# Kernel tuning notes

Hardware: AMD Instinct MI355X
Metric: run time of the kernel (lower is better)

The kernel has to match this reference:

```python
import jax, jax.numpy as jnp
import numpy as np

DIM = 512
H = 8
D = 64
EPS = 1e-5


def _ln(x, g, b):
    m = jnp.mean(x, axis=-1, keepdims=True)
    v = jnp.var(x, axis=-1, keepdims=True)
    return (x - m) * jax.lax.rsqrt(v + EPS) * g + b


def _attn(x, ctx, wq, wk, wv, wo, bo):
    B, S, _ = x.shape
    T = ctx.shape[1]
    q = (x @ wq).reshape(B, S, H, D)
    k = (ctx @ wk).reshape(B, T, H, D)
    v = (ctx @ wv).reshape(B, T, H, D)
    scale = D ** -0.5
    score = jnp.einsum('bqhd,bkhd->bhqk', q, k) * scale  # [B,H,S,T]
    w = jax.nn.softmax(score, axis=-1)
    o = jnp.einsum('bhqk,bkhd->bqhd', w, v).reshape(B, S, H * D)
    return o @ wo + bo


def _geglu(x, w, b):
    h = x @ w + b
    y, gate = h[..., :4 * DIM], h[..., 4 * DIM:]
    tanh_res = jnp.tanh(gate * 0.7978845608 * (1.0 + 0.044715 * gate * gate))
    return y * 0.5 * gate * (1.0 + tanh_res)


def setup_inputs() -> dict:
    key = jax.random.key(0)
    ks = jax.random.split(key, 16)
    s = 0.02
    inp = {
        'x': jax.random.normal(ks[0], (2, 4096, DIM), jnp.float32),
        'context': jax.random.normal(ks[1], (2, 77, DIM), jnp.float32),
        'ln1_g': jnp.ones((DIM,), jnp.float32),
        'ln1_b': jnp.zeros((DIM,), jnp.float32),
        'wq1': jax.random.normal(ks[2], (DIM, H * D), jnp.float32) * s,
        'wk1': jax.random.normal(ks[3], (DIM, H * D), jnp.float32) * s,
        'wv1': jax.random.normal(ks[4], (DIM, H * D), jnp.float32) * s,
        'wo1': jax.random.normal(ks[5], (H * D, H * D), jnp.float32) * s,
        'bo1': jnp.zeros((H * D,), jnp.float32),
        'ln2_g': jnp.ones((DIM,), jnp.float32),
        'ln2_b': jnp.zeros((DIM,), jnp.float32),
        'wq2': jax.random.normal(ks[6], (DIM, H * D), jnp.float32) * s,
        'wk2': jax.random.normal(ks[7], (DIM, H * D), jnp.float32) * s,
        'wv2': jax.random.normal(ks[8], (DIM, H * D), jnp.float32) * s,
        'wo2': jax.random.normal(ks[9], (H * D, H * D), jnp.float32) * s,
        'bo2': jnp.zeros((H * D,), jnp.float32),
        'ln3_g': jnp.ones((DIM,), jnp.float32),
        'ln3_b': jnp.zeros((DIM,), jnp.float32),
        'geglu_w': jax.random.normal(ks[10], (DIM, 8 * DIM), jnp.float32) * s,
        'geglu_b': jnp.zeros((8 * DIM,), jnp.float32),
        'out_w': jax.random.normal(ks[11], (4 * DIM, DIM), jnp.float32) * s,
        'out_b': jnp.zeros((DIM,), jnp.float32),
    }
    return inp


def reference(x, context, ln1_g, ln1_b, wq1, wk1, wv1, wo1, bo1,
              ln2_g, ln2_b, wq2, wk2, wv2, wo2, bo2,
              ln3_g, ln3_b, geglu_w, geglu_b, out_w, out_b):
    h = _attn(_ln(x, ln1_g, ln1_b), _ln(x, ln1_g, ln1_b), wq1, wk1, wv1, wo1, bo1) + x
    h = _attn(_ln(h, ln2_g, ln2_b), context, wq2, wk2, wv2, wo2, bo2) + h
    ff = _geglu(_ln(h, ln3_g, ln3_b), geglu_w, geglu_b)
    return ff @ out_w + out_b + h
```

## Files before the change

kernel.cpp:

```cpp
#include <hip/hip_runtime.h>
#include <hip/hip_bf16.h>
#include <math.h>

#define DIM 512
#define NHEAD 8
#define HD 64
#define BATCH 2
#define SEQ 4096
#define CTXLEN 77
#define NTOK (BATCH*SEQ)
#define NCTX (BATCH*CTXLEN)

typedef __hip_bfloat16 bf16;
typedef __attribute__((ext_vector_type(8))) short bf8_t;
typedef __attribute__((ext_vector_type(4))) float f4_t;

__device__ __forceinline__ float b2f(bf16 v){ return __bfloat162float(v); }
__device__ __forceinline__ bf16  f2b(float v){ return __float2bfloat16(v); }
__device__ __forceinline__ unsigned short f2bu(float v){ bf16 h = f2b(v); return *(unsigned short*)&h; }
__device__ __forceinline__ unsigned int packbf2(float a, float b){
    return (unsigned int)f2bu(a) | ((unsigned int)f2bu(b) << 16);
}
__device__ __forceinline__ void  stf(float* p, float v){ *p = v; }
__device__ __forceinline__ void  stf(bf16* p, float v){ *p = f2b(v); }

__global__ __launch_bounds__(256)
void ln_kernel(const float* __restrict__ x, const float* __restrict__ g,
               const float* __restrict__ b, bf16* __restrict__ out, int nrows)
{
    int row  = blockIdx.x * 4 + (threadIdx.x >> 6);
    int lane = threadIdx.x & 63;
    if (row >= nrows) return;
    const float* xr = x + (size_t)row * DIM;
    float v[8];
    float s = 0.f, sq = 0.f;
    #pragma unroll
    for (int j = 0; j < 8; ++j) {
        float f = xr[lane + 64*j];
        v[j] = f; s += f; sq += f*f;
    }
    #pragma unroll
    for (int off = 32; off; off >>= 1) {
        s  += __shfl_xor(s,  off);
        sq += __shfl_xor(sq, off);
    }
    float mean = s * (1.f/DIM);
    float var  = sq * (1.f/DIM) - mean*mean;
    float rstd = rsqrtf(var + 1e-5f);
    bf16* orow = out + (size_t)row * DIM;
    #pragma unroll
    for (int j = 0; j < 8; ++j) {
        int c = lane + 64*j;
        orow[c] = f2b((v[j]-mean)*rstd*g[c] + b[c]);
    }
}

__global__ __launch_bounds__(256)
void transpose_bf16_kernel(const float* __restrict__ W, bf16* __restrict__ Wt, int K, int N)
{
    __shared__ float tile[32][33];
    int n0 = blockIdx.x * 32, k0 = blockIdx.y * 32;
    int tx = threadIdx.x & 31, ty = threadIdx.x >> 5;
    #pragma unroll
    for (int p = 0; p < 4; ++p)
        tile[ty + p*8][tx] = W[(size_t)(k0 + ty + p*8)*N + n0 + tx];
    __syncthreads();
    #pragma unroll
    for (int p = 0; p < 4; ++p)
        Wt[(size_t)(n0 + ty + p*8)*K + k0 + tx] = f2b(tile[tx][ty + p*8]);
}

struct TPtrs { const float* src[8]; bf16* dst[8]; };
__global__ __launch_bounds__(256)
void transpose8_kernel(TPtrs p)
{
    __shared__ float tile[32][33];
    const float* W = p.src[blockIdx.z];
    bf16* Wt = p.dst[blockIdx.z];
    int n0 = blockIdx.x * 32, k0 = blockIdx.y * 32;
    int tx = threadIdx.x & 31, ty = threadIdx.x >> 5;
    #pragma unroll
    for (int q = 0; q < 4; ++q)
        tile[ty + q*8][tx] = W[(size_t)(k0 + ty + q*8)*512 + n0 + tx];
    __syncthreads();
    #pragma unroll
    for (int q = 0; q < 4; ++q)
        Wt[(size_t)(n0 + ty + q*8)*512 + k0 + tx] = f2b(tile[tx][ty + q*8]);
}

__global__ __launch_bounds__(256)
void cast_bf16_kernel(const float* __restrict__ in, bf16* __restrict__ out, int n)
{
    int i = blockIdx.x*256 + threadIdx.x;
    if (i < n) out[i] = f2b(in[i]);
}

__global__ __launch_bounds__(256)
void v_transpose_kernel(const bf16* __restrict__ V, bf16* __restrict__ Vt, int T, int pitch)
{
    __shared__ __align__(16) unsigned short tile[64*64];
    const int tid = threadIdx.x;
    const int b = blockIdx.z, h = blockIdx.y;
    const int t0 = blockIdx.x * 64;
    #pragma unroll
    for (int it = 0; it < 2; ++it) {
        int e = tid + it*256;
        int t = e >> 3, c = e & 7;
        int gk = t0 + t;
        bf8_t v = {0,0,0,0,0,0,0,0};
        if (gk < T) v = *(const bf8_t*)(V + ((size_t)(b*T + gk))*DIM + h*HD + c*8);
        *(bf8_t*)&tile[t*64 + c*8] = v;
    }
    __syncthreads();
    #pragma unroll
    for (int it = 0; it < 2; ++it) {
        int e = tid + it*256;
        int d = e & 63, oc = e >> 6;
        unsigned short tmp[8];
        #pragma unroll
        for (int j = 0; j < 8; ++j) tmp[j] = tile[(oc*8 + j)*64 + d];
        *(bf8_t*)(Vt + ((size_t)((b*8 + h)*64 + d))*pitch + t0 + oc*8) = *(bf8_t*)tmp;
    }
}

struct OutPtrs { void* p[3]; };
template<int RESID, typename OUTT, bool GUARD>
__global__ __launch_bounds__(256)
void gemm_mfma_kernel(const bf16* __restrict__ A, const bf16* __restrict__ Wt,
                      const float* __restrict__ bias, const float* __restrict__ resid,
                      OutPtrs outs, int M, int K)
{
    __shared__ __align__(16) unsigned short As[128*64];
    __shared__ __align__(16) unsigned short Bs[64*64];
    const int tid  = threadIdx.x;
    const int wave = tid >> 6, lane = tid & 63;
    const int l16  = lane & 15, quad = lane >> 4;
    const int wm = (wave >> 1) * 64, wn = (wave & 1) * 32;
    const int m0 = blockIdx.y * 128, n0 = blockIdx.x * 64;
    OUTT* outp = (OUTT*)outs.p[n0 >> 9];
    const int lc0 = n0 & 511;

    f4_t acc[4][2];
    #pragma unroll
    for (int i = 0; i < 4; ++i) { acc[i][0] = f4_t{0,0,0,0}; acc[i][1] = f4_t{0,0,0,0}; }

    for (int k0 = 0; k0 < K; k0 += 64) {
        #pragma unroll
        for (int p = 0; p < 4; ++p) {
            int e = tid + p*256;
            int r = e >> 3, c = e & 7;
            int gr = m0 + r;
            if (GUARD) gr = (gr < M) ? gr : (M-1);
            bf8_t v = *(const bf8_t*)(A + (size_t)gr*K + k0 + c*8);
            *(bf8_t*)&As[r*64 + ((c ^ (r&7))*8)] = v;
        }
        #pragma unroll
        for (int p = 0; p < 2; ++p) {
            int e = tid + p*256;
            int r = e >> 3, c = e & 7;
            bf8_t v = *(const bf8_t*)(Wt + (size_t)(n0 + r)*K + k0 + c*8);
            *(bf8_t*)&Bs[r*64 + ((c ^ (r&7))*8)] = v;
        }
        __syncthreads();
        #pragma unroll
        for (int kc = 0; kc < 2; ++kc) {
            const int cg = kc*4 + quad;
            bf8_t af[4], bfr[2];
            #pragma unroll
            for (int mt = 0; mt < 4; ++mt) {
                int r = wm + mt*16 + l16;
                af[mt] = *(const bf8_t*)&As[r*64 + ((cg ^ (r&7))*8)];
            }
            #pragma unroll
            for (int nt = 0; nt < 2; ++nt) {
                int r = wn + nt*16 + l16;
                bfr[nt] = *(const bf8_t*)&Bs[r*64 + ((cg ^ (r&7))*8)];
            }
            #pragma unroll
            for (int mt = 0; mt < 4; ++mt)
                #pragma unroll
                for (int nt = 0; nt < 2; ++nt)
                    acc[mt][nt] = __builtin_amdgcn_mfma_f32_16x16x32_bf16(af[mt], bfr[nt], acc[mt][nt], 0, 0, 0);
        }
        __syncthreads();
    }

    #pragma unroll
    for (int mt = 0; mt < 4; ++mt) {
        #pragma unroll
        for (int r_ = 0; r_ < 4; ++r_) {
            int row = m0 + wm + mt*16 + quad*4 + r_;
            if (GUARD && row >= M) continue;
            size_t rb = (size_t)row * 512;
            #pragma unroll
            for (int nt = 0; nt < 2; ++nt) {
                int col = lc0 + wn + nt*16 + l16;
                float v = acc[mt][nt][r_];
                if (bias) v += bias[col];
                if (RESID) v += resid[rb + col];
                stf(&outp[rb + col], v);
            }
        }
    }
}

__global__ __launch_bounds__(256)
void geglu_mfma_kernel(const bf16* __restrict__ A, const bf16* __restrict__ WtG,
                       const float* __restrict__ bias, bf16* __restrict__ outp)
{
    __shared__ __align__(16) unsigned short As[128*64];
    __shared__ __align__(16) unsigned short Bys[64*64];
    __shared__ __align__(16) unsigned short Bgs[64*64];
    const int tid  = threadIdx.x;
    const int wave = tid >> 6, lane = tid & 63;
    const int l16  = lane & 15, quad = lane >> 4;
    const int m0 = blockIdx.y * 128, n0 = blockIdx.x * 64;
    const int srow = tid >> 3, scol = tid & 7;

    f4_t accy[2][4], accg[2][4];
    #pragma unroll
    for (int i = 0; i < 2; ++i)
        #pragma unroll
        for (int j = 0; j < 4; ++j) { accy[i][j] = f4_t{0,0,0,0}; accg[i][j] = f4_t{0,0,0,0}; }

    for (int k0 = 0; k0 < DIM; k0 += 64) {
        #pragma unroll
        for (int p = 0; p < 4; ++p) {
            int r = srow + p*32;
            bf8_t v = *(const bf8_t*)(A + (size_t)(m0 + r)*DIM + k0 + scol*8);
            *(bf8_t*)&As[r*64 + ((scol ^ (r&7))*8)] = v;
        }
        #pragma unroll
        for (int p = 0; p < 2; ++p) {
            int r = srow + p*32;
            bf8_t vy = *(const bf8_t*)(WtG + (size_t)(n0 + r)*DIM + k0 + scol*8);
            bf8_t vg = *(const bf8_t*)(WtG + (size_t)(2048 + n0 + r)*DIM + k0 + scol*8);
            *(bf8_t*)&Bys[r*64 + ((scol ^ (r&7))*8)] = vy;
            *(bf8_t*)&Bgs[r*64 + ((scol ^ (r&7))*8)] = vg;
        }
        __syncthreads();
        #pragma unroll
        for (int kc = 0; kc < 2; ++kc) {
            const int cg = kc*4 + quad;
            bf8_t af[2];
            #pragma unroll
            for (int mt = 0; mt < 2; ++mt) {
                int r = wave*32 + mt*16 + l16;
                af[mt] = *(const bf8_t*)&As[r*64 + ((cg ^ (r&7))*8)];
            }
            #pragma unroll
            for (int nt = 0; nt < 4; ++nt) {
                int r = nt*16 + l16;
                bf8_t by = *(const bf8_t*)&Bys[r*64 + ((cg ^ (r&7))*8)];
                bf8_t bg = *(const bf8_t*)&Bgs[r*64 + ((cg ^ (r&7))*8)];
                #pragma unroll
                for (int mt = 0; mt < 2; ++mt) {
                    accy[mt][nt] = __builtin_amdgcn_mfma_f32_16x16x32_bf16(af[mt], by, accy[mt][nt], 0, 0, 0);
                    accg[mt][nt] = __builtin_amdgcn_mfma_f32_16x16x32_bf16(af[mt], bg, accg[mt][nt], 0, 0, 0);
                }
            }
        }
        __syncthreads();
    }

    #pragma unroll
    for (int mt = 0; mt < 2; ++mt) {
        #pragma unroll
        for (int r_ = 0; r_ < 4; ++r_) {
            int row = m0 + wave*32 + mt*16 + quad*4 + r_;
            size_t rb = (size_t)row * 2048;
            #pragma unroll
            for (int nt = 0; nt < 4; ++nt) {
                int col = n0 + nt*16 + l16;
                float y = accy[mt][nt][r_] + bias[col];
                float g = accg[mt][nt][r_] + bias[2048 + col];
                float t = tanhf(0.7978845608f*g*(1.f + 0.044715f*g*g));
                outp[rb + col] = f2b(y * 0.5f * g * (1.f + t));
            }
        }
    }
}

__global__ __launch_bounds__(256)
void attn_mfma_kernel(const bf16* __restrict__ Qm, const bf16* __restrict__ Km,
                      const bf16* __restrict__ VtG, bf16* __restrict__ Om,
                      int T, int vpitch)
{
    __shared__ __align__(16) unsigned short Ks[64*64];
    __shared__ __align__(16) unsigned short Vts[64*64];
    __shared__ __align__(16) unsigned short Ps[4][16*64];

    const int tid  = threadIdx.x;
    const int wave = tid >> 6, lane = tid & 63;
    const int l16  = lane & 15, quad = lane >> 4;
    const int b = blockIdx.z, h = blockIdx.y;
    const int qblk = blockIdx.x * 128;

    bf8_t qf[2][2];
    #pragma unroll
    for (int qn = 0; qn < 2; ++qn) {
        const bf16* qp = Qm + ((size_t)(b*SEQ + qblk + wave*32 + qn*16 + l16))*DIM + h*HD + quad*8;
        #pragma unroll
        for (int kc = 0; kc < 2; ++kc) {
            bf8_t v = *(const bf8_t*)(qp + kc*32);
            unsigned short* u = (unsigned short*)&v;
            #pragma unroll
            for (int j = 0; j < 8; ++j) {
                bf16 hv = *(bf16*)&u[j];
                u[j] = f2bu(b2f(hv) * 0.125f);
            }
            qf[qn][kc] = v;
        }
    }

    f4_t o[4][2];
    #pragma unroll
    for (int dt = 0; dt < 4; ++dt) { o[dt][0] = f4_t{0,0,0,0}; o[dt][1] = f4_t{0,0,0,0}; }
    float m_run[2] = {-1e30f, -1e30f}, l_run[2] = {0.f, 0.f};

    const int ntiles = (T + 63) >> 6;
    for (int t0 = 0; t0 < ntiles; ++t0) {
        const int kb = t0 << 6;
        #pragma unroll
        for (int it = 0; it < 2; ++it) {
            int e = tid + it*256;
            int r = e >> 3, c = e & 7;
            int gk = kb + r;
            bf8_t kv = {0,0,0,0,0,0,0,0};
            if (gk < T) kv = *(const bf8_t*)(Km + ((size_t)(b*T + gk))*DIM + h*HD + c*8);
            *(bf8_t*)&Ks[r*64 + ((c ^ (r&7))*8)] = kv;
            bf8_t vv = *(const bf8_t*)(VtG + ((size_t)((b*8 + h)*64 + r))*vpitch + kb + c*8);
            *(bf8_t*)&Vts[r*64 + ((c ^ (r&7))*8)] = vv;
        }
        __syncthreads();

        bf8_t kf[4][2], vf[4][2];
        #pragma unroll
        for (int t = 0; t < 4; ++t) {
            int r = t*16 + l16;
            #pragma unroll
            for (int kc = 0; kc < 2; ++kc) {
                int cg = kc*4 + quad;
                kf[t][kc] = *(const bf8_t*)&Ks[r*64 + ((cg ^ (r&7))*8)];
                vf[t][kc] = *(const bf8_t*)&Vts[r*64 + ((cg ^ (r&7))*8)];
            }
        }
        const bool tail = (kb + 64 > T);

        #pragma unroll
        for (int qn = 0; qn < 2; ++qn) {
            f4_t sc[4];
            #pragma unroll
            for (int km = 0; km < 4; ++km) {
                f4_t c = {0,0,0,0};
                c = __builtin_amdgcn_mfma_f32_16x16x32_bf16(kf[km][0], qf[qn][0], c, 0, 0, 0);
                c = __builtin_amdgcn_mfma_f32_16x16x32_bf16(kf[km][1], qf[qn][1], c, 0, 0, 0);
                sc[km] = c;
            }
            if (tail) {
                #pragma unroll
                for (int km = 0; km < 4; ++km)
                    #pragma unroll
                    for (int r = 0; r < 4; ++r)
                        if (kb + km*16 + quad*4 + r >= T) sc[km][r] = -1e30f;
            }
            float mx = sc[0][0];
            #pragma unroll
            for (int km = 0; km < 4; ++km)
                #pragma unroll
                for (int r = 0; r < 4; ++r) mx = fmaxf(mx, sc[km][r]);
            mx = fmaxf(mx, __shfl_xor(mx, 16));
            mx = fmaxf(mx, __shfl_xor(mx, 32));
            float mnew = fmaxf(m_run[qn], mx);
            float psum = 0.f;
            #pragma unroll
            for (int km = 0; km < 4; ++km)
                #pragma unroll
                for (int r = 0; r < 4; ++r) {
                    float p = __expf(sc[km][r] - mnew);
                    sc[km][r] = p; psum += p;
                }
            psum += __shfl_xor(psum, 16);
            psum += __shfl_xor(psum, 32);
            float alpha = __expf(m_run[qn] - mnew);
            m_run[qn] = mnew;
            l_run[qn] = l_run[qn]*alpha + psum;
            #pragma unroll
            for (int dt = 0; dt < 4; ++dt)
                #pragma unroll
                for (int r = 0; r < 4; ++r) o[dt][qn][r] *= alpha;
            #pragma unroll
            for (int km = 0; km < 4; ++km) {
                uint2 w;
                w.x = packbf2(sc[km][0], sc[km][1]);
                w.y = packbf2(sc[km][2], sc[km][3]);
                int chunk = 2*km + (quad >> 1);
                int a = l16*64 + ((chunk ^ (l16 & 7))*8) + (quad & 1)*4;
                *(uint2*)&Ps[wave][a] = w;
            }
            #pragma unroll
            for (int kc = 0; kc < 2; ++kc) {
                int cg = kc*4 + quad;
                bf8_t pf = *(const bf8_t*)&Ps[wave][l16*64 + ((cg ^ (l16 & 7))*8)];
                #pragma unroll
                for (int dt = 0; dt < 4; ++dt)
                    o[dt][qn] = __builtin_amdgcn_mfma_f32_16x16x32_bf16(vf[dt][kc], pf, o[dt][qn], 0, 0, 0);
            }
        }
        __syncthreads();
    }

    #pragma unroll
    for (int qn = 0; qn < 2; ++qn) {
        float inv = 1.f / l_run[qn];
        int tok = qblk + wave*32 + qn*16 + l16;
        size_t base = ((size_t)(b*SEQ + tok))*DIM + h*HD;
        #pragma unroll
        for (int dt = 0; dt < 4; ++dt) {
            uint2 w;
            w.x = packbf2(o[dt][qn][0]*inv, o[dt][qn][1]*inv);
            w.y = packbf2(o[dt][qn][2]*inv, o[dt][qn][3]*inv);
            *(uint2*)(Om + base + dt*16 + quad*4) = w;
        }
    }
}

extern "C" void kernel_launch(void* const* d_in, const int* in_sizes, int n_in,
                              void* d_out, int out_size, void* d_ws, size_t ws_size,
                              hipStream_t stream)
{
    (void)in_sizes; (void)n_in; (void)out_size; (void)ws_size;
    const float* x    = (const float*)d_in[0];
    const float* ctx  = (const float*)d_in[1];
    const float* ln1g = (const float*)d_in[2];
    const float* ln1b = (const float*)d_in[3];
    const float* wq1  = (const float*)d_in[4];
    const float* wk1  = (const float*)d_in[5];
    const float* wv1  = (const float*)d_in[6];
    const float* wo1  = (const float*)d_in[7];
    const float* bo1  = (const float*)d_in[8];
    const float* ln2g = (const float*)d_in[9];
    const float* ln2b = (const float*)d_in[10];
    const float* wq2  = (const float*)d_in[11];
    const float* wk2  = (const float*)d_in[12];
    const float* wv2  = (const float*)d_in[13];
    const float* wo2  = (const float*)d_in[14];
    const float* bo2  = (const float*)d_in[15];
    const float* ln3g = (const float*)d_in[16];
    const float* ln3b = (const float*)d_in[17];
    const float* gw   = (const float*)d_in[18];
    const float* gb   = (const float*)d_in[19];
    const float* ow   = (const float*)d_in[20];
    const float* ob   = (const float*)d_in[21];
    float* out = (float*)d_out;

    char* ws = (char*)d_ws;
    bf16* An  = (bf16*)(ws);
    bf16* VtG = (bf16*)(ws);
    bf16* Qb  = (bf16*)(ws + ((size_t)8<<20));
    bf16* Kb  = (bf16*)(ws + ((size_t)16<<20));
    bf16* Vb  = (bf16*)(ws + ((size_t)24<<20));
    bf16* Ob  = (bf16*)(ws + ((size_t)32<<20));
    bf16* FF  = Qb;
    float* Hf = out;
    bf16* WT  = (bf16*)(ws + ((size_t)40<<20));
    bf16* wq1T = WT + 0*262144, *wk1T = WT + 1*262144, *wv1T = WT + 2*262144, *wo1T = WT + 3*262144;
    bf16* wq2T = WT + 4*262144, *wk2T = WT + 5*262144, *wv2T = WT + 6*262144, *wo2T = WT + 7*262144;
    bf16* gwT  = (bf16*)(ws + ((size_t)44<<20));
    bf16* owT  = (bf16*)(ws + ((size_t)48<<20));
    bf16* ctxb = (bf16*)(ws + ((size_t)50<<20));
    bf16* VtG2 = (bf16*)(ws + ((size_t)50<<20) + ((size_t)512<<10));

    dim3 blk(256);

    TPtrs tp;
    tp.src[0]=wq1; tp.src[1]=wk1; tp.src[2]=wv1; tp.src[3]=wo1;
    tp.src[4]=wq2; tp.src[5]=wk2; tp.src[6]=wv2; tp.src[7]=wo2;
    tp.dst[0]=wq1T; tp.dst[1]=wk1T; tp.dst[2]=wv1T; tp.dst[3]=wo1T;
    tp.dst[4]=wq2T; tp.dst[5]=wk2T; tp.dst[6]=wv2T; tp.dst[7]=wo2T;
    transpose8_kernel<<<dim3(16,16,8), blk, 0, stream>>>(tp);
    transpose_bf16_kernel<<<dim3(128,16), blk, 0, stream>>>(gw, gwT, DIM, 4096);
    transpose_bf16_kernel<<<dim3(16,64), blk, 0, stream>>>(ow, owT, 2048, DIM);
    cast_bf16_kernel<<<dim3((NCTX*DIM+255)/256), blk, 0, stream>>>(ctx, ctxb, NCTX*DIM);

    dim3 gLN(NTOK/4);
    dim3 gQKV(24, 64);
    dim3 gG(8, 64);
    dim3 gKVx(16, 2);
    dim3 gGEGLU(32, 64);
    dim3 gATT(SEQ/128, NHEAD, BATCH);
    OutPtrs oQKV{{Qb, Kb, Vb}};
    OutPtrs oKVx{{Kb, Vb, nullptr}};
    OutPtrs oQ{{Qb, nullptr, nullptr}};
    OutPtrs oH{{Hf, nullptr, nullptr}};
    OutPtrs oOut{{out, nullptr, nullptr}};
    OutPtrs oOb{{Ob, nullptr, nullptr}};

    ln_kernel<<<gLN, blk, 0, stream>>>(x, ln1g, ln1b, An, NTOK);
    gemm_mfma_kernel<0,bf16,false><<<gQKV, blk, 0, stream>>>(An, wq1T, nullptr, nullptr, oQKV, NTOK, DIM);
    v_transpose_kernel<<<dim3(SEQ/64, NHEAD, BATCH), blk, 0, stream>>>(Vb, VtG, SEQ, SEQ);
    attn_mfma_kernel<<<gATT, blk, 0, stream>>>(Qb, Kb, VtG, Ob, SEQ, SEQ);
    gemm_mfma_kernel<1,float,false><<<gG, blk, 0, stream>>>(Ob, wo1T, bo1, x, oH, NTOK, DIM);

    ln_kernel<<<gLN, blk, 0, stream>>>(Hf, ln2g, ln2b, An, NTOK);
    gemm_mfma_kernel<0,bf16,false><<<gG, blk, 0, stream>>>(An, wq2T, nullptr, nullptr, oQ, NTOK, DIM);
    gemm_mfma_kernel<0,bf16,true><<<gKVx, blk, 0, stream>>>(ctxb, wk2T, nullptr, nullptr, oKVx, NCTX, DIM);
    v_transpose_kernel<<<dim3(2, NHEAD, BATCH), blk, 0, stream>>>(Vb, VtG2, CTXLEN, 128);
    attn_mfma_kernel<<<gATT, blk, 0, stream>>>(Qb, Kb, VtG2, Ob, CTXLEN, 128);
    gemm_mfma_kernel<1,float,false><<<gG, blk, 0, stream>>>(Ob, wo2T, bo2, Hf, oH, NTOK, DIM);

    ln_kernel<<<gLN, blk, 0, stream>>>(Hf, ln3g, ln3b, An, NTOK);
    geglu_mfma_kernel<<<gGEGLU, blk, 0, stream>>>(An, gwT, gb, FF);
    gemm_mfma_kernel<1,float,false><<<gG, blk, 0, stream>>>(FF, owT, ob, Hf, oOut, NTOK, 2048);
}
```

Measured before the change: 549.3 us.

## Split self-attention over two key halves and merge partial softmax results

The self-attention kernel now splits the key range into two halves, doubling the grid so more blocks run across the CUs. Each half writes bf16 partial outputs plus per-row running max and sum into workspace, and a new merge kernel combines them with rescaled weights. Separately, log2(e) is folded into the query scale so exp2f replaces __expf. The cost is an extra kernel launch, extra global traffic for the partials and max/sum values, and some added bf16 rounding from the intermediate partial outputs.

```diff
diff --git a/kernel.cpp b/kernel.cpp
--- a/kernel.cpp
+++ b/kernel.cpp
@@ -281,10 +281,11 @@
     }
 }
 
+template<bool FINAL>
 __global__ __launch_bounds__(256)
 void attn_mfma_kernel(const bf16* __restrict__ Qm, const bf16* __restrict__ Km,
                       const bf16* __restrict__ VtG, bf16* __restrict__ Om,
-                      int T, int vpitch)
+                      float2* __restrict__ ml, int T, int vpitch)
 {
     __shared__ __align__(16) unsigned short Ks[64*64];
     __shared__ __align__(16) unsigned short Vts[64*64];
@@ -293,7 +294,11 @@
     const int tid  = threadIdx.x;
     const int wave = tid >> 6, lane = tid & 63;
     const int l16  = lane & 15, quad = lane >> 4;
-    const int b = blockIdx.z, h = blockIdx.y;
+    const int z = blockIdx.z, h = blockIdx.y;
+    const int b = FINAL ? z : (z >> 1);
+    const int s = FINAL ? 0 : (z & 1);
+    const int kstart = FINAL ? 0 : s*(SEQ/2);
+    const int kend   = FINAL ? T : kstart + SEQ/2;
     const int qblk = blockIdx.x * 128;
 
     bf8_t qf[2][2];
@@ -307,7 +312,7 @@
             #pragma unroll
             for (int j = 0; j < 8; ++j) {
                 bf16 hv = *(bf16*)&u[j];
-                u[j] = f2bu(b2f(hv) * 0.125f);
+                u[j] = f2bu(b2f(hv) * 0.1803368801f);
             }
             qf[qn][kc] = v;
         }
@@ -318,9 +323,7 @@
     for (int dt = 0; dt < 4; ++dt) { o[dt][0] = f4_t{0,0,0,0}; o[dt][1] = f4_t{0,0,0,0}; }
     float m_run[2] = {-1e30f, -1e30f}, l_run[2] = {0.f, 0.f};
 
-    const int ntiles = (T + 63) >> 6;
-    for (int t0 = 0; t0 < ntiles; ++t0) {
-        const int kb = t0 << 6;
+    for (int kb = kstart; kb < kend; kb += 64) {
         #pragma unroll
         for (int it = 0; it < 2; ++it) {
             int e = tid + it*256;
@@ -377,12 +380,12 @@
             for (int km = 0; km < 4; ++km)
                 #pragma unroll
                 for (int r = 0; r < 4; ++r) {
-                    float p = __expf(sc[km][r] - mnew);
+                    float p = exp2f(sc[km][r] - mnew);
                     sc[km][r] = p; psum += p;
                 }
             psum += __shfl_xor(psum, 16);
             psum += __shfl_xor(psum, 32);
-            float alpha = __expf(m_run[qn] - mnew);
+            float alpha = exp2f(m_run[qn] - mnew);
             m_run[qn] = mnew;
             l_run[qn] = l_run[qn]*alpha + psum;
             #pragma unroll
@@ -410,6 +413,7 @@
         __syncthreads();
     }
 
+    bf16* Ob_ = FINAL ? Om : (Om + (size_t)s * NTOK * DIM);
     #pragma unroll
     for (int qn = 0; qn < 2; ++qn) {
         float inv = 1.f / l_run[qn];
@@ -420,9 +424,39 @@
             uint2 w;
             w.x = packbf2(o[dt][qn][0]*inv, o[dt][qn][1]*inv);
             w.y = packbf2(o[dt][qn][2]*inv, o[dt][qn][3]*inv);
-            *(uint2*)(Om + base + dt*16 + quad*4) = w;
-        }
-    }
+            *(uint2*)(Ob_ + base + dt*16 + quad*4) = w;
+        }
+        if (!FINAL && quad == 0)
+            ml[((size_t)(z*NHEAD + h))*SEQ + tok] = make_float2(m_run[qn], l_run[qn]);
+    }
+}
+
+__global__ __launch_bounds__(256)
+void attn_merge_kernel(const bf16* __restrict__ P, const float2* __restrict__ ml,
+                       bf16* __restrict__ Out)
+{
+    int idx = blockIdx.x*256 + threadIdx.x;
+    int tok = idx >> 6;
+    int c = idx & 63, h = c >> 3, dc = c & 7;
+    int b = tok >> 12, stok = tok & 4095;
+    float2 ml0 = ml[((size_t)((b*2+0)*NHEAD + h))*SEQ + stok];
+    float2 ml1 = ml[((size_t)((b*2+1)*NHEAD + h))*SEQ + stok];
+    float m = fmaxf(ml0.x, ml1.x);
+    float a0 = exp2f(ml0.x - m) * ml0.y;
+    float a1 = exp2f(ml1.x - m) * ml1.y;
+    float inv = 1.f / (a0 + a1);
+    a0 *= inv; a1 *= inv;
+    size_t off = (size_t)tok*DIM + h*HD + dc*8;
+    bf8_t v0 = *(const bf8_t*)(P + off);
+    bf8_t v1 = *(const bf8_t*)(P + (size_t)NTOK*DIM + off);
+    unsigned short r[8];
+    #pragma unroll
+    for (int j = 0; j < 8; ++j) {
+        float f0 = b2f(*(bf16*)&((unsigned short*)&v0)[j]);
+        float f1 = b2f(*(bf16*)&((unsigned short*)&v1)[j]);
+        r[j] = f2bu(a0*f0 + a1*f1);
+    }
+    *(bf8_t*)(Out + off) = *(bf8_t*)r;
 }
 
 extern "C" void kernel_launch(void* const* d_in, const int* in_sizes, int n_in,
@@ -470,6 +504,7 @@
     bf16* owT  = (bf16*)(ws + ((size_t)48<<20));
     bf16* ctxb = (bf16*)(ws + ((size_t)50<<20));
     bf16* VtG2 = (bf16*)(ws + ((size_t)50<<20) + ((size_t)512<<10));
+    float2* mlbuf = (float2*)(ws + ((size_t)51<<20));
 
     dim3 blk(256);
 
@@ -488,25 +523,26 @@
     dim3 gG(8, 64);
     dim3 gKVx(16, 2);
     dim3 gGEGLU(32, 64);
-    dim3 gATT(SEQ/128, NHEAD, BATCH);
+    dim3 gATTs(SEQ/128, NHEAD, BATCH*2);
+    dim3 gATTx(SEQ/128, NHEAD, BATCH);
     OutPtrs oQKV{{Qb, Kb, Vb}};
     OutPtrs oKVx{{Kb, Vb, nullptr}};
     OutPtrs oQ{{Qb, nullptr, nullptr}};
     OutPtrs oH{{Hf, nullptr, nullptr}};
     OutPtrs oOut{{out, nullptr, nullptr}};
-    OutPtrs oOb{{Ob, nullptr, nullptr}};
 
     ln_kernel<<<gLN, blk, 0, stream>>>(x, ln1g, ln1b, An, NTOK);
     gemm_mfma_kernel<0,bf16,false><<<gQKV, blk, 0, stream>>>(An, wq1T, nullptr, nullptr, oQKV, NTOK, DIM);
     v_transpose_kernel<<<dim3(SEQ/64, NHEAD, BATCH), blk, 0, stream>>>(Vb, VtG, SEQ, SEQ);
-    attn_mfma_kernel<<<gATT, blk, 0, stream>>>(Qb, Kb, VtG, Ob, SEQ, SEQ);
-    gemm_mfma_kernel<1,float,false><<<gG, blk, 0, stream>>>(Ob, wo1T, bo1, x, oH, NTOK, DIM);
+    attn_mfma_kernel<false><<<gATTs, blk, 0, stream>>>(Qb, Kb, VtG, Vb, mlbuf, SEQ, SEQ);
+    attn_merge_kernel<<<dim3(NTOK*NHEAD*8/256), blk, 0, stream>>>(Vb, mlbuf, Qb);
+    gemm_mfma_kernel<1,float,false><<<gG, blk, 0, stream>>>(Qb, wo1T, bo1, x, oH, NTOK, DIM);
 
     ln_kernel<<<gLN, blk, 0, stream>>>(Hf, ln2g, ln2b, An, NTOK);
     gemm_mfma_kernel<0,bf16,false><<<gG, blk, 0, stream>>>(An, wq2T, nullptr, nullptr, oQ, NTOK, DIM);
     gemm_mfma_kernel<0,bf16,true><<<gKVx, blk, 0, stream>>>(ctxb, wk2T, nullptr, nullptr, oKVx, NCTX, DIM);
     v_transpose_kernel<<<dim3(2, NHEAD, BATCH), blk, 0, stream>>>(Vb, VtG2, CTXLEN, 128);
-    attn_mfma_kernel<<<gATT, blk, 0, stream>>>(Qb, Kb, VtG2, Ob, CTXLEN, 128);
+    attn_mfma_kernel<true><<<gATTx, blk, 0, stream>>>(Qb, Kb, VtG2, Ob, nullptr, CTXLEN, 128);
     gemm_mfma_kernel<1,float,false><<<gG, blk, 0, stream>>>(Ob, wo2T, bo2, Hf, oH, NTOK, DIM);
 
     ln_kernel<<<gLN, blk, 0, stream>>>(Hf, ln3g, ln3b, An, NTOK);
```

After: 578.2 us. 1.05x slower.

## Process 128-key tiles with two independent softmax streams and exp2 scaling

Applied to the files above, without the earlier changes.

The attention kernel now loads 128 keys per iteration and splits them into two 64-key subtiles. Each subtile keeps its own running max, sum and output accumulator, and the two are merged in a final rescale. This halves the number of block barriers and gives the scheduler two independent MFMA/softmax chains. The query scale now folds in log2(e) so exp2f can replace __expf. In exchange, LDS use doubles and accumulator registers grow, which may lower occupancy, and V fragments are now read from LDS inside the PV loop instead of being preloaded.

```diff
diff --git a/kernel.cpp b/kernel.cpp
--- a/kernel.cpp
+++ b/kernel.cpp
@@ -286,9 +286,9 @@
                       const bf16* __restrict__ VtG, bf16* __restrict__ Om,
                       int T, int vpitch)
 {
-    __shared__ __align__(16) unsigned short Ks[64*64];
-    __shared__ __align__(16) unsigned short Vts[64*64];
-    __shared__ __align__(16) unsigned short Ps[4][16*64];
+    __shared__ __align__(16) unsigned short Ks[128*64];
+    __shared__ __align__(16) unsigned short Vts[64*128];
+    __shared__ __align__(16) unsigned short Ps[2][4][16*64];
 
     const int tid  = threadIdx.x;
     const int wave = tid >> 6, lane = tid & 63;
@@ -307,104 +307,116 @@
             #pragma unroll
             for (int j = 0; j < 8; ++j) {
                 bf16 hv = *(bf16*)&u[j];
-                u[j] = f2bu(b2f(hv) * 0.125f);
+                u[j] = f2bu(b2f(hv) * 0.1803368801f);
             }
             qf[qn][kc] = v;
         }
     }
 
-    f4_t o[4][2];
-    #pragma unroll
-    for (int dt = 0; dt < 4; ++dt) { o[dt][0] = f4_t{0,0,0,0}; o[dt][1] = f4_t{0,0,0,0}; }
-    float m_run[2] = {-1e30f, -1e30f}, l_run[2] = {0.f, 0.f};
-
-    const int ntiles = (T + 63) >> 6;
-    for (int t0 = 0; t0 < ntiles; ++t0) {
-        const int kb = t0 << 6;
-        #pragma unroll
-        for (int it = 0; it < 2; ++it) {
-            int e = tid + it*256;
+    f4_t o[2][4][2];
+    float m_run[2][2], l_run[2][2];
+    #pragma unroll
+    for (int st = 0; st < 2; ++st) {
+        #pragma unroll
+        for (int dt = 0; dt < 4; ++dt) { o[st][dt][0] = f4_t{0,0,0,0}; o[st][dt][1] = f4_t{0,0,0,0}; }
+        m_run[st][0] = -1e30f; m_run[st][1] = -1e30f;
+        l_run[st][0] = 0.f;    l_run[st][1] = 0.f;
+    }
+
+    const int kend = ((T + 63) >> 6) << 6;
+    for (int kb = 0; kb < kend; kb += 128) {
+        #pragma unroll
+        for (int p = 0; p < 4; ++p) {
+            int e = tid + p*256;
             int r = e >> 3, c = e & 7;
             int gk = kb + r;
             bf8_t kv = {0,0,0,0,0,0,0,0};
             if (gk < T) kv = *(const bf8_t*)(Km + ((size_t)(b*T + gk))*DIM + h*HD + c*8);
             *(bf8_t*)&Ks[r*64 + ((c ^ (r&7))*8)] = kv;
+        }
+        #pragma unroll
+        for (int p = 0; p < 4; ++p) {
+            int e = tid + p*256;
+            int r = e >> 4, c = e & 15;
             bf8_t vv = *(const bf8_t*)(VtG + ((size_t)((b*8 + h)*64 + r))*vpitch + kb + c*8);
-            *(bf8_t*)&Vts[r*64 + ((c ^ (r&7))*8)] = vv;
+            *(bf8_t*)&Vts[r*128 + ((c ^ (r&15))*8)] = vv;
         }
         __syncthreads();
 
-        bf8_t kf[4][2], vf[4][2];
-        #pragma unroll
-        for (int t = 0; t < 4; ++t) {
-            int r = t*16 + l16;
-            #pragma unroll
-            for (int kc = 0; kc < 2; ++kc) {
-                int cg = kc*4 + quad;
-                kf[t][kc] = *(const bf8_t*)&Ks[r*64 + ((cg ^ (r&7))*8)];
-                vf[t][kc] = *(const bf8_t*)&Vts[r*64 + ((cg ^ (r&7))*8)];
-            }
-        }
-        const bool tail = (kb + 64 > T);
-
-        #pragma unroll
-        for (int qn = 0; qn < 2; ++qn) {
-            f4_t sc[4];
+        #pragma unroll
+        for (int st = 0; st < 2; ++st) {
+            bf8_t kf[4][2];
             #pragma unroll
             for (int km = 0; km < 4; ++km) {
-                f4_t c = {0,0,0,0};
-                c = __builtin_amdgcn_mfma_f32_16x16x32_bf16(kf[km][0], qf[qn][0], c, 0, 0, 0);
-                c = __builtin_amdgcn_mfma_f32_16x16x32_bf16(kf[km][1], qf[qn][1], c, 0, 0, 0);
-                sc[km] = c;
-            }
-            if (tail) {
+                int r = st*64 + km*16 + l16;
+                #pragma unroll
+                for (int kc = 0; kc < 2; ++kc)
+                    kf[km][kc] = *(const bf8_t*)&Ks[r*64 + (((kc*4 + quad) ^ (r&7))*8)];
+            }
+            const bool tail = (kb + st*64 + 64 > T);
+
+            #pragma unroll
+            for (int qn = 0; qn < 2; ++qn) {
+                f4_t sc[4];
+                #pragma unroll
+                for (int km = 0; km < 4; ++km) {
+                    f4_t c = {0,0,0,0};
+                    c = __builtin_amdgcn_mfma_f32_16x16x32_bf16(kf[km][0], qf[qn][0], c, 0, 0, 0);
+                    c = __builtin_amdgcn_mfma_f32_16x16x32_bf16(kf[km][1], qf[qn][1], c, 0, 0, 0);
+                    sc[km] = c;
+                }
+                if (tail) {
+                    #pragma unroll
+                    for (int km = 0; km < 4; ++km)
+                        #pragma unroll
+                        for (int r = 0; r < 4; ++r)
+                            if (kb + st*64 + km*16 + quad*4 + r >= T) sc[km][r] = -1e30f;
+                }
+                float mx = sc[0][0];
                 #pragma unroll
                 for (int km = 0; km < 4; ++km)
                     #pragma unroll
-                    for (int r = 0; r < 4; ++r)
-                        if (kb + km*16 + quad*4 + r >= T) sc[km][r] = -1e30f;
-            }
-            float mx = sc[0][0];
-            #pragma unroll
-            for (int km = 0; km < 4; ++km)
-                #pragma unroll
-                for (int r = 0; r < 4; ++r) mx = fmaxf(mx, sc[km][r]);
-            mx = fmaxf(mx, __shfl_xor(mx, 16));
-            mx = fmaxf(mx, __shfl_xor(mx, 32));
-            float mnew = fmaxf(m_run[qn], mx);
-            float psum = 0.f;
-            #pragma unroll
-            for (int km = 0; km < 4; ++km)
-                #pragma unroll
-                for (int r = 0; r < 4; ++r) {
-                    float p = __expf(sc[km][r] - mnew);
-                    sc[km][r] = p; psum += p;
+                    for (int r = 0; r < 4; ++r) mx = fmaxf(mx, sc[km][r]);
+                mx = fmaxf(mx, __shfl_xor(mx, 16));
+                mx = fmaxf(mx, __shfl_xor(mx, 32));
+                float mnew = fmaxf(m_run[st][qn], mx);
+                float psum = 0.f;
+                #pragma unroll
+                for (int km = 0; km < 4; ++km)
+                    #pragma unroll
+                    for (int r = 0; r < 4; ++r) {
+                        float p = exp2f(sc[km][r] - mnew);
+                        sc[km][r] = p; psum += p;
+                    }
+                psum += __shfl_xor(psum, 16);
+                psum += __shfl_xor(psum, 32);
+                float alpha = exp2f(m_run[st][qn] - mnew);
+                m_run[st][qn] = mnew;
+                l_run[st][qn] = l_run[st][qn]*alpha + psum;
+                #pragma unroll
+                for (int dt = 0; dt < 4; ++dt)
+                    #pragma unroll
+                    for (int r = 0; r < 4; ++r) o[st][dt][qn][r] *= alpha;
+                #pragma unroll
+                for (int km = 0; km < 4; ++km) {
+                    uint2 w;
+                    w.x = packbf2(sc[km][0], sc[km][1]);
+                    w.y = packbf2(sc[km][2], sc[km][3]);
+                    int chunk = 2*km + (quad >> 1);
+                    int a = l16*64 + ((chunk ^ (l16 & 7))*8) + (quad & 1)*4;
+                    *(uint2*)&Ps[st][wave][a] = w;
                 }
-            psum += __shfl_xor(psum, 16);
-            psum += __shfl_xor(psum, 32);
-            float alpha = __expf(m_run[qn] - mnew);
-            m_run[qn] = mnew;
-            l_run[qn] = l_run[qn]*alpha + psum;
-            #pragma unroll
-            for (int dt = 0; dt < 4; ++dt)
-                #pragma unroll
-                for (int r = 0; r < 4; ++r) o[dt][qn][r] *= alpha;
-            #pragma unroll
-            for (int km = 0; km < 4; ++km) {
-                uint2 w;
-                w.x = packbf2(sc[km][0], sc[km][1]);
-                w.y = packbf2(sc[km][2], sc[km][3]);
-                int chunk = 2*km + (quad >> 1);
-                int a = l16*64 + ((chunk ^ (l16 & 7))*8) + (quad & 1)*4;
-                *(uint2*)&Ps[wave][a] = w;
-            }
-            #pragma unroll
-            for (int kc = 0; kc < 2; ++kc) {
-                int cg = kc*4 + quad;
-                bf8_t pf = *(const bf8_t*)&Ps[wave][l16*64 + ((cg ^ (l16 & 7))*8)];
-                #pragma unroll
-                for (int dt = 0; dt < 4; ++dt)
-                    o[dt][qn] = __builtin_amdgcn_mfma_f32_16x16x32_bf16(vf[dt][kc], pf, o[dt][qn], 0, 0, 0);
+                #pragma unroll
+                for (int kc = 0; kc < 2; ++kc) {
+                    bf8_t pf = *(const bf8_t*)&Ps[st][wave][l16*64 + (((kc*4 + quad) ^ (l16 & 7))*8)];
+                    #pragma unroll
+                    for (int dt = 0; dt < 4; ++dt) {
+                        int vr = dt*16 + l16;
+                        int vc = st*8 + kc*4 + quad;
+                        bf8_t vf = *(const bf8_t*)&Vts[vr*128 + ((vc ^ (vr&15))*8)];
+                        o[st][dt][qn] = __builtin_amdgcn_mfma_f32_16x16x32_bf16(vf, pf, o[st][dt][qn], 0, 0, 0);
+                    }
+                }
             }
         }
         __syncthreads();
@@ -412,14 +424,22 @@
 
     #pragma unroll
     for (int qn = 0; qn < 2; ++qn) {
-        float inv = 1.f / l_run[qn];
+        float mA = m_run[0][qn], mB = m_run[1][qn];
+        float m = fmaxf(mA, mB);
+        float cA = exp2f(mA - m), cB = exp2f(mB - m);
+        float inv = 1.f / (l_run[0][qn]*cA + l_run[1][qn]*cB);
+        cA *= inv; cB *= inv;
         int tok = qblk + wave*32 + qn*16 + l16;
         size_t base = ((size_t)(b*SEQ + tok))*DIM + h*HD;
         #pragma unroll
         for (int dt = 0; dt < 4; ++dt) {
+            float v0 = o[0][dt][qn][0]*cA + o[1][dt][qn][0]*cB;
+            float v1 = o[0][dt][qn][1]*cA + o[1][dt][qn][1]*cB;
+            float v2 = o[0][dt][qn][2]*cA + o[1][dt][qn][2]*cB;
+            float v3 = o[0][dt][qn][3]*cA + o[1][dt][qn][3]*cB;
             uint2 w;
-            w.x = packbf2(o[dt][qn][0]*inv, o[dt][qn][1]*inv);
-            w.y = packbf2(o[dt][qn][2]*inv, o[dt][qn][3]*inv);
+            w.x = packbf2(v0, v1);
+            w.y = packbf2(v2, v3);
             *(uint2*)(Om + base + dt*16 + quad*4) = w;
         }
     }
@@ -494,7 +514,6 @@
     OutPtrs oQ{{Qb, nullptr, nullptr}};
     OutPtrs oH{{Hf, nullptr, nullptr}};
     OutPtrs oOut{{out, nullptr, nullptr}};
-    OutPtrs oOb{{Ob, nullptr, nullptr}};
 
     ln_kernel<<<gLN, blk, 0, stream>>>(x, ln1g, ln1b, An, NTOK);
     gemm_mfma_kernel<0,bf16,false><<<gQKV, blk, 0, stream>>>(An, wq1T, nullptr, nullptr, oQKV, NTOK, DIM);
```

Result: slower. 683.1 us (+24.3%).
